# Optimization experiments

Hardware: AMD Instinct MI355X
Metric: run time of the kernel (lower is better)

## Reference

```python
import jax, jax.numpy as jnp
import numpy as np

B = 128          # batch of codewords
M_CHK = 288      # n_check_nodes
N_VAR = 576      # n_variable_nodes
K_INFO = 288     # n_information_bits
N_ITER = 5
EDGE_P = 0.02    # ~11-12 edges per check row, LDPC-like sparsity


def setup_inputs() -> dict:
    key = jax.random.key(0)
    k1, k2, k3, k4 = jax.random.split(key, 4)
    inputs = jax.random.normal(k1, (B, N_VAR), dtype=jnp.float32)
    # sparse binary parity-check matrix, batched (keras RNN constants carry batch dim)
    H = jax.random.bernoulli(k2, EDGE_P, (B, M_CHK, N_VAR)).astype(jnp.float32)
    sigma2 = 0.5 + 0.5 * jax.random.uniform(k3, (B, 1), dtype=jnp.float32)
    # learned parameters
    input_ponderation = jnp.ones((N_ITER, 1), dtype=jnp.float32)
    out_ponderation = jnp.ones((N_ITER, 1), dtype=jnp.float32)
    skip_ponderation = jnp.ones((1, 1), dtype=jnp.float32)
    # per-edge check-to-variable weights of the neural BP cell
    w_cv = 1.0 + 0.02 * jax.random.normal(k4, (M_CHK, N_VAR), dtype=jnp.float32)
    gate_logit = jnp.asarray(0.0, dtype=jnp.float32)
    return {"inputs": inputs, "H": H, "sigma2": sigma2,
            "input_ponderation": input_ponderation,
            "out_ponderation": out_ponderation,
            "skip_ponderation": skip_ponderation,
            "w_cv": w_cv, "gate_logit": gate_logit}


def _decode(inputs, H, sigma2, input_ponderation, out_ponderation,
            skip_ponderation, w_cv, gate_logit):
    llrs = -4.0 * inputs / sigma2                                    # [B, n]
    # trainable=True path: normalize by mean |llr|
    norm_llrs = llrs / jnp.mean(jnp.abs(llrs), axis=-1, keepdims=True)
    # tile over iterations and apply input ponderation -> [B, T, n]
    x = norm_llrs[:, None, :] * input_ponderation

    mask = H                                                         # [B, m, n]
    gate = jax.nn.sigmoid(gate_logit)

    def cell(Mstate, x_t):
        # variable-to-check extrinsic messages on edges
        S = jnp.sum(Mstate, axis=1, keepdims=True)                   # [B, 1, n]
        V = (x_t[:, None, :] + S - Mstate) * mask                    # [B, m, n]
        # tanh-product check-node update (product excluding self via divide)
        t = jnp.tanh(0.5 * jnp.clip(V, -15.0, 15.0))
        t_edge = jnp.where(mask > 0, t, 1.0)
        P = jnp.prod(t_edge, axis=-1, keepdims=True)                 # [B, m, 1]
        t_safe = jnp.where(jnp.abs(t_edge) < 1e-7,
                           jnp.where(t_edge >= 0, 1e-7, -1e-7), t_edge)
        r = jnp.clip(P / t_safe, -1.0 + 1e-6, 1.0 - 1e-6)
        M_new = 2.0 * jnp.arctanh(r) * w_cv * mask                   # weighted c2v
        # gated (damped) state update
        M_out = gate * M_new + (1.0 - gate) * Mstate
        posterior = x_t + jnp.sum(M_out, axis=1)                     # [B, n]
        return M_out, posterior

    M0 = jnp.zeros_like(H)
    xs = jnp.swapaxes(x, 0, 1)                                       # [T, B, n]
    _, posts = jax.lax.scan(cell, M0, xs)
    outputs = jnp.swapaxes(posts, 0, 1)                              # [B, T, n]

    # post-normalization per iteration, weighted pooling over iterations
    norm_out = outputs / jnp.mean(jnp.abs(outputs), axis=-1, keepdims=True)
    pooled = jnp.mean(out_ponderation * norm_out, axis=-2)           # [B, n]
    out = pooled + skip_ponderation * norm_llrs                      # [1,1] broadcast
    return jax.nn.sigmoid(-out[:, :K_INFO])


def reference(inputs, H, sigma2, input_ponderation, out_ponderation,
              skip_ponderation, w_cv, gate_logit):
    return _decode(inputs, H, sigma2, input_ponderation, out_ponderation,
                   skip_ponderation, w_cv, gate_logit)
```

## Files before the change

kernel.cpp:

```cpp
#include <hip/hip_runtime.h>

#define B_SZ  128
#define MCHK  288
#define NVAR  576
#define KINFO 288
#define NITER 5
#define ECAP  3712
#define CAP2  32
#define TPB   1024
#define NQ4   (MCHK * NVAR / 4)
#define Q4ROW (NVAR / 4)

__global__ __launch_bounds__(TPB) void decode(
    const float* __restrict__ inp,   const float* __restrict__ H,
    const float* __restrict__ sigma2,const float* __restrict__ ipond,
    const float* __restrict__ opond, const float* __restrict__ skipp,
    const float* __restrict__ wcv,   const float* __restrict__ gatel,
    float* __restrict__ out)
{
    __shared__ float Mld[ECAP];
    __shared__ float tld[ECAP];
    __shared__ float wld[ECAP];
    __shared__ unsigned int ev[ECAP];
    __shared__ float Sb[NITER + 1][NVAR];
    __shared__ float xln[NVAR];
    __shared__ float Prow[MCHK];
    __shared__ int   rcnt[MCHK], roff[MCHK];
    __shared__ unsigned short vpad[MCHK * CAP2];
    __shared__ float red[NITER * 16];
    __shared__ float scalv[NITER];
    __shared__ int   wtot[8], wbase[8];

    const int b    = blockIdx.x;
    const int tid  = threadIdx.x;
    const int wid  = tid >> 6;
    const int lane = tid & 63;

    const float sig  = sigma2[b];
    const float gate = 1.0f / (1.0f + __expf(-gatel[0]));
    const float gbar = 1.0f - gate;

    float ipl[NITER], opl[NITER];
    #pragma unroll
    for (int t = 0; t < NITER; ++t) { ipl[t] = ipond[t]; opl[t] = opond[t]; }

    float l = 0.0f, al = 0.0f, xv = 0.0f;
    if (tid < NVAR) { l = -4.0f * inp[(size_t)b * NVAR + tid] / sig; al = fabsf(l); }
    #pragma unroll
    for (int o = 32; o; o >>= 1) al += __shfl_down(al, o, 64);
    if (lane == 0) red[wid] = al;
    if (tid < MCHK) rcnt[tid] = 0;
    for (int i = tid; i < (NITER + 1) * NVAR; i += TPB) ((float*)Sb)[i] = 0.0f;
    __syncthreads();
    if (wid == 0) {
        float s = (lane < 16) ? red[lane] : 0.0f;
        s += __shfl_down(s, 8, 64); s += __shfl_down(s, 4, 64);
        s += __shfl_down(s, 2, 64); s += __shfl_down(s, 1, 64);
        if (lane == 0) scalv[0] = (float)NVAR / s;
    }
    __syncthreads();
    if (tid < NVAR) { xv = l * scalv[0]; xln[tid] = xv; }

    {
        const float4* H4 = (const float4*)(H + (size_t)b * MCHK * NVAR);
        for (int k = 0; k < (NQ4 + TPB - 1) / TPB; ++k) {
            int q = tid + k * TPB;
            if (q >= NQ4) break;
            float4 hv = H4[q];
            if (hv.x != 0.f || hv.y != 0.f || hv.z != 0.f || hv.w != 0.f) {
                int r  = q / Q4ROW;
                int c0 = (q - r * Q4ROW) * 4;
                unsigned short* vp = vpad + r * CAP2;
                if (hv.x != 0.f) { int j = atomicAdd(&rcnt[r], 1); if (j < CAP2) vp[j] = (unsigned short)(c0);     }
                if (hv.y != 0.f) { int j = atomicAdd(&rcnt[r], 1); if (j < CAP2) vp[j] = (unsigned short)(c0 + 1); }
                if (hv.z != 0.f) { int j = atomicAdd(&rcnt[r], 1); if (j < CAP2) vp[j] = (unsigned short)(c0 + 2); }
                if (hv.w != 0.f) { int j = atomicAdd(&rcnt[r], 1); if (j < CAP2) vp[j] = (unsigned short)(c0 + 3); }
            }
        }
    }
    __syncthreads();

    int cc = 0, incl = 0;
    if (tid < 512) {
        cc = (tid < MCHK) ? rcnt[tid] : 0;
        if (cc > CAP2) cc = CAP2;
        incl = cc;
        #pragma unroll
        for (int o = 1; o < 64; o <<= 1) {
            int n = __shfl_up(incl, o, 64);
            if (lane >= o) incl += n;
        }
        if (lane == 63) wtot[wid] = incl;
    }
    __syncthreads();
    if (tid == 0) {
        int s = 0;
        #pragma unroll
        for (int i = 0; i < 8; ++i) { wbase[i] = s; s += wtot[i]; }
    }
    __syncthreads();
    if (tid < MCHK) {
        int o = incl + wbase[wid] - cc;
        int ce = cc;
        if (o >= ECAP)           { o = 0; ce = 0; }
        else if (o + ce > ECAP)  { ce = ECAP - o; }
        roff[tid] = o; rcnt[tid] = ce;
    }
    const int Etot = wbase[7] + wtot[7];
    const int E    = (Etot > ECAP) ? ECAP : Etot;
    __syncthreads();

    for (int s = tid; s < MCHK * CAP2; s += TPB) {
        int r = s >> 5, j = s & (CAP2 - 1);
        if (j < rcnt[r]) {
            int e   = roff[r] + j;
            int col = vpad[s];
            ev[e]  = ((unsigned)r << 16) | (unsigned)col;
            wld[e] = wcv[r * NVAR + col];
            Mld[e] = 0.0f;
        }
    }
    __syncthreads();

    for (int t = 0; t < NITER; ++t) {
        const float pt = ipl[t];
        const float* St = Sb[t];
        float*       Sn = Sb[t + 1];

        for (int e = tid; e < E; e += TPB) {
            int v   = (int)(ev[e] & 0xFFFFu);
            float V = fmaf(pt, xln[v], St[v]) - Mld[e];
            V = fminf(15.0f, fmaxf(-15.0f, V));
            float ex = __expf(V);
            float te = (ex - 1.0f) * __builtin_amdgcn_rcpf(ex + 1.0f);
            float x  = 0.5f * V, x2 = x * x;
            float tp = x * fmaf(x2, fmaf(x2, fmaf(x2, -0.05396825f, 0.13333333f),
                                         -0.33333333f), 1.0f);
            tld[e] = (fabsf(V) < 0.5f) ? tp : te;
        }
        __syncthreads();

        if (tid < MCHK) {
            int o = roff[tid], oe = o + rcnt[tid];
            float p0 = 1.0f, p1 = 1.0f, p2 = 1.0f, p3 = 1.0f;
            int j = o;
            for (; j + 4 <= oe; j += 4) {
                float t0 = tld[j], t1 = tld[j + 1], t2 = tld[j + 2], t3 = tld[j + 3];
                p0 *= t0; p1 *= t1; p2 *= t2; p3 *= t3;
            }
            for (; j < oe; ++j) p0 *= tld[j];
            Prow[tid] = (p0 * p1) * (p2 * p3);
        }
        __syncthreads();

        for (int e = tid; e < E; e += TPB) {
            unsigned pk = ev[e];
            int v = (int)(pk & 0xFFFFu);
            int r = (int)(pk >> 16);
            float tj = tld[e];
            float ts = (fabsf(tj) < 1e-7f) ? ((tj >= 0.0f) ? 1e-7f : -1e-7f) : tj;
            float rr = Prow[r] * __builtin_amdgcn_rcpf(ts);
            rr = fminf(1.0f - 1e-6f, fmaxf(-1.0f + 1e-6f, rr));
            float Mn = __logf((1.0f + rr) * __builtin_amdgcn_rcpf(1.0f - rr)) * wld[e];
            float Mo = fmaf(gate, Mn, gbar * Mld[e]);
            Mld[e] = Mo;
            atomicAdd(&Sn[v], Mo);
        }
        __syncthreads();
    }

    float ap[NITER] = {0, 0, 0, 0, 0};
    if (tid < NVAR) {
        #pragma unroll
        for (int t = 0; t < NITER; ++t)
            ap[t] = fabsf(fmaf(ipl[t], xv, Sb[t + 1][tid]));
    }
    #pragma unroll
    for (int o = 32; o; o >>= 1) {
        #pragma unroll
        for (int t = 0; t < NITER; ++t) ap[t] += __shfl_down(ap[t], o, 64);
    }
    if (lane == 0) {
        #pragma unroll
        for (int t = 0; t < NITER; ++t) red[t * 16 + wid] = ap[t];
    }
    __syncthreads();
    if (wid == 0) {
        #pragma unroll
        for (int t = 0; t < NITER; ++t) {
            float s = (lane < 16) ? red[t * 16 + lane] : 0.0f;
            s += __shfl_down(s, 8, 64); s += __shfl_down(s, 4, 64);
            s += __shfl_down(s, 2, 64); s += __shfl_down(s, 1, 64);
            if (lane == 0) scalv[t] = (float)NVAR / s;
        }
    }
    __syncthreads();
    if (tid < KINFO) {
        float acc = 0.0f;
        #pragma unroll
        for (int t = 0; t < NITER; ++t)
            acc += opl[t] * fmaf(ipl[t], xv, Sb[t + 1][tid]) * scalv[t];
        float o = acc * (1.0f / NITER) + skipp[0] * xv;
        out[(size_t)b * KINFO + tid] = 1.0f / (1.0f + __expf(o));
    }
}

extern "C" void kernel_launch(void* const* d_in, const int* in_sizes, int n_in,
                              void* d_out, int out_size, void* d_ws, size_t ws_size,
                              hipStream_t stream) {
    const float* inp    = (const float*)d_in[0];
    const float* H      = (const float*)d_in[1];
    const float* sigma2 = (const float*)d_in[2];
    const float* ipond  = (const float*)d_in[3];
    const float* opond  = (const float*)d_in[4];
    const float* skipp  = (const float*)d_in[5];
    const float* wcv    = (const float*)d_in[6];
    const float* gatel  = (const float*)d_in[7];
    float* out = (float*)d_out;

    decode<<<B_SZ, TPB, 0, stream>>>(inp, H, sigma2, ipond, opond, skipp,
                                     wcv, gatel, out);
}
```

Measured before the change: 189.2 us.

## Split sparse edge extraction into wide kernel and use log-domain row products

Moves the dense scan of H (the dominant memory read) out of the 128-block decoder into a separate extraction kernel launched with 16 blocks per codeword, which writes compact edge lists to workspace. Edges of each row are no longer contiguous, so the per-row tanh product is computed in the log domain with shared-memory atomics for the log-magnitude sum and the negative-sign count. The extrinsic product is then recovered by exp2 of a difference, which replaces the serial per-row product loop and a barrier. This adds a memset, an extra launch, a global round-trip for the edges and atomic contention, and log-domain rounding differs slightly from the direct division.

```diff
diff --git a/kernel.cpp b/kernel.cpp
--- a/kernel.cpp
+++ b/kernel.cpp
@@ -5,31 +5,103 @@
 #define NVAR  576
 #define KINFO 288
 #define NITER 5
-#define ECAP  3712
+#define EPAD  4096
+#define RPB   18
+#define XBLK  (MCHK / RPB)
 #define CAP2  32
 #define TPB   1024
-#define NQ4   (MCHK * NVAR / 4)
-#define Q4ROW (NVAR / 4)
+
+__device__ __forceinline__ void scat(float4 hv, int q, int* rc,
+                                     unsigned short* vpad) {
+    if (hv.x != 0.f || hv.y != 0.f || hv.z != 0.f || hv.w != 0.f) {
+        int r  = q / (NVAR / 4);
+        int c0 = (q - r * (NVAR / 4)) * 4;
+        unsigned short* vp = vpad + r * CAP2;
+        if (hv.x != 0.f) { int j = atomicAdd(&rc[r], 1); if (j < CAP2) vp[j] = (unsigned short)(c0);     }
+        if (hv.y != 0.f) { int j = atomicAdd(&rc[r], 1); if (j < CAP2) vp[j] = (unsigned short)(c0 + 1); }
+        if (hv.z != 0.f) { int j = atomicAdd(&rc[r], 1); if (j < CAP2) vp[j] = (unsigned short)(c0 + 2); }
+        if (hv.w != 0.f) { int j = atomicAdd(&rc[r], 1); if (j < CAP2) vp[j] = (unsigned short)(c0 + 3); }
+    }
+}
+
+__global__ __launch_bounds__(256) void extract(
+    const float* __restrict__ H, const float* __restrict__ wcv,
+    int* __restrict__ eCnt, unsigned int* __restrict__ evG,
+    float* __restrict__ wG)
+{
+    __shared__ unsigned short vpad[RPB * CAP2];
+    __shared__ int rc[RPB], ro[RPB];
+    __shared__ int baseS;
+
+    const int b    = blockIdx.x >> 4;
+    const int g    = blockIdx.x & 15;
+    const int tid  = threadIdx.x;
+    const int row0 = g * RPB;
+
+    if (tid < RPB) rc[tid] = 0;
+    __syncthreads();
+
+    const float4* H4 = (const float4*)(H + ((size_t)b * MCHK + row0) * NVAR);
+    #pragma unroll
+    for (int k0 = 0; k0 < 8; k0 += 4) {
+        int q0 = tid + k0 * 256;
+        float4 h0 = H4[q0], h1 = H4[q0 + 256], h2 = H4[q0 + 512], h3 = H4[q0 + 768];
+        scat(h0, q0, rc, vpad);       scat(h1, q0 + 256, rc, vpad);
+        scat(h2, q0 + 512, rc, vpad); scat(h3, q0 + 768, rc, vpad);
+    }
+    {
+        int q0 = tid + 8 * 256;
+        float4 h0 = H4[q0], h1 = H4[q0 + 256];
+        scat(h0, q0, rc, vpad); scat(h1, q0 + 256, rc, vpad);
+    }
+    if (tid < 32) { int q = tid + 2560; scat(H4[q], q, rc, vpad); }
+    __syncthreads();
+
+    if (tid < 64) {
+        int c = (tid < RPB) ? ((rc[tid] > CAP2) ? CAP2 : rc[tid]) : 0;
+        int incl = c;
+        #pragma unroll
+        for (int o = 1; o < 64; o <<= 1) {
+            int n = __shfl_up(incl, o, 64);
+            if (tid >= o) incl += n;
+        }
+        if (tid < RPB) { ro[tid] = incl - c; rc[tid] = c; }
+        int tot = __shfl(incl, RPB - 1, 64);
+        if (tid == 0) baseS = atomicAdd(&eCnt[b], tot);
+    }
+    __syncthreads();
+    const int base = baseS;
+    for (int s = tid; s < RPB * CAP2; s += 256) {
+        int r = s >> 5, j = s & 31;
+        if (j < rc[r]) {
+            int e = base + ro[r] + j;
+            if (e < EPAD) {
+                int col  = vpad[s];
+                int grow = row0 + r;
+                evG[(size_t)b * EPAD + e] = ((unsigned)grow << 16) | (unsigned)col;
+                wG [(size_t)b * EPAD + e] = wcv[grow * NVAR + col];
+            }
+        }
+    }
+}
 
 __global__ __launch_bounds__(TPB) void decode(
-    const float* __restrict__ inp,   const float* __restrict__ H,
-    const float* __restrict__ sigma2,const float* __restrict__ ipond,
-    const float* __restrict__ opond, const float* __restrict__ skipp,
-    const float* __restrict__ wcv,   const float* __restrict__ gatel,
-    float* __restrict__ out)
+    const float* __restrict__ inp,   const float* __restrict__ sigma2,
+    const float* __restrict__ ipond, const float* __restrict__ opond,
+    const float* __restrict__ skipp, const float* __restrict__ gatel,
+    const int* __restrict__ eCnt,    const unsigned int* __restrict__ evG,
+    const float* __restrict__ wG,    float* __restrict__ out)
 {
-    __shared__ float Mld[ECAP];
-    __shared__ float tld[ECAP];
-    __shared__ float wld[ECAP];
-    __shared__ unsigned int ev[ECAP];
+    __shared__ unsigned int ev[EPAD];
+    __shared__ float wld[EPAD];
+    __shared__ float Mld[EPAD];
+    __shared__ float pld[EPAD];
     __shared__ float Sb[NITER + 1][NVAR];
     __shared__ float xln[NVAR];
-    __shared__ float Prow[MCHK];
-    __shared__ int   rcnt[MCHK], roff[MCHK];
-    __shared__ unsigned short vpad[MCHK * CAP2];
+    __shared__ float Plog[2][MCHK];
+    __shared__ int   Png [2][MCHK];
     __shared__ float red[NITER * 16];
     __shared__ float scalv[NITER];
-    __shared__ int   wtot[8], wbase[8];
 
     const int b    = blockIdx.x;
     const int tid  = threadIdx.x;
@@ -49,8 +121,18 @@
     #pragma unroll
     for (int o = 32; o; o >>= 1) al += __shfl_down(al, o, 64);
     if (lane == 0) red[wid] = al;
-    if (tid < MCHK) rcnt[tid] = 0;
     for (int i = tid; i < (NITER + 1) * NVAR; i += TPB) ((float*)Sb)[i] = 0.0f;
+    if (tid < 2 * MCHK) { ((float*)Plog)[tid] = 0.0f; ((int*)Png)[tid] = 0; }
+
+    const int E = min(eCnt[b], EPAD);
+    #pragma unroll
+    for (int k = 0; k < EPAD / TPB; ++k) {
+        int j = tid + k * TPB;
+        unsigned e = ((unsigned)MCHK << 16);
+        float w = 0.0f;
+        if (j < E) { e = evG[(size_t)b * EPAD + j]; w = wG[(size_t)b * EPAD + j]; }
+        ev[j] = e; wld[j] = w; Mld[j] = 0.0f;
+    }
     __syncthreads();
     if (wid == 0) {
         float s = (lane < 16) ? red[lane] : 0.0f;
@@ -60,112 +142,61 @@
     }
     __syncthreads();
     if (tid < NVAR) { xv = l * scalv[0]; xln[tid] = xv; }
-
-    {
-        const float4* H4 = (const float4*)(H + (size_t)b * MCHK * NVAR);
-        for (int k = 0; k < (NQ4 + TPB - 1) / TPB; ++k) {
-            int q = tid + k * TPB;
-            if (q >= NQ4) break;
-            float4 hv = H4[q];
-            if (hv.x != 0.f || hv.y != 0.f || hv.z != 0.f || hv.w != 0.f) {
-                int r  = q / Q4ROW;
-                int c0 = (q - r * Q4ROW) * 4;
-                unsigned short* vp = vpad + r * CAP2;
-                if (hv.x != 0.f) { int j = atomicAdd(&rcnt[r], 1); if (j < CAP2) vp[j] = (unsigned short)(c0);     }
-                if (hv.y != 0.f) { int j = atomicAdd(&rcnt[r], 1); if (j < CAP2) vp[j] = (unsigned short)(c0 + 1); }
-                if (hv.z != 0.f) { int j = atomicAdd(&rcnt[r], 1); if (j < CAP2) vp[j] = (unsigned short)(c0 + 2); }
-                if (hv.w != 0.f) { int j = atomicAdd(&rcnt[r], 1); if (j < CAP2) vp[j] = (unsigned short)(c0 + 3); }
-            }
-        }
-    }
-    __syncthreads();
-
-    int cc = 0, incl = 0;
-    if (tid < 512) {
-        cc = (tid < MCHK) ? rcnt[tid] : 0;
-        if (cc > CAP2) cc = CAP2;
-        incl = cc;
-        #pragma unroll
-        for (int o = 1; o < 64; o <<= 1) {
-            int n = __shfl_up(incl, o, 64);
-            if (lane >= o) incl += n;
-        }
-        if (lane == 63) wtot[wid] = incl;
-    }
-    __syncthreads();
-    if (tid == 0) {
-        int s = 0;
-        #pragma unroll
-        for (int i = 0; i < 8; ++i) { wbase[i] = s; s += wtot[i]; }
-    }
-    __syncthreads();
-    if (tid < MCHK) {
-        int o = incl + wbase[wid] - cc;
-        int ce = cc;
-        if (o >= ECAP)           { o = 0; ce = 0; }
-        else if (o + ce > ECAP)  { ce = ECAP - o; }
-        roff[tid] = o; rcnt[tid] = ce;
-    }
-    const int Etot = wbase[7] + wtot[7];
-    const int E    = (Etot > ECAP) ? ECAP : Etot;
-    __syncthreads();
-
-    for (int s = tid; s < MCHK * CAP2; s += TPB) {
-        int r = s >> 5, j = s & (CAP2 - 1);
-        if (j < rcnt[r]) {
-            int e   = roff[r] + j;
-            int col = vpad[s];
-            ev[e]  = ((unsigned)r << 16) | (unsigned)col;
-            wld[e] = wcv[r * NVAR + col];
-            Mld[e] = 0.0f;
-        }
-    }
     __syncthreads();
 
     for (int t = 0; t < NITER; ++t) {
+        const int cur = t & 1, nxt = cur ^ 1;
         const float pt = ipl[t];
         const float* St = Sb[t];
         float*       Sn = Sb[t + 1];
 
-        for (int e = tid; e < E; e += TPB) {
-            int v   = (int)(ev[e] & 0xFFFFu);
-            float V = fmaf(pt, xln[v], St[v]) - Mld[e];
-            V = fminf(15.0f, fmaxf(-15.0f, V));
-            float ex = __expf(V);
-            float te = (ex - 1.0f) * __builtin_amdgcn_rcpf(ex + 1.0f);
-            float x  = 0.5f * V, x2 = x * x;
-            float tp = x * fmaf(x2, fmaf(x2, fmaf(x2, -0.05396825f, 0.13333333f),
-                                         -0.33333333f), 1.0f);
-            tld[e] = (fabsf(V) < 0.5f) ? tp : te;
+        #pragma unroll
+        for (int k = 0; k < EPAD / TPB; ++k) {
+            int e = tid + k * TPB;
+            unsigned pk = ev[e];
+            int r = (int)(pk >> 16);
+            if (r < MCHK) {
+                int v = (int)(pk & 0xFFFFu);
+                float V = fmaf(pt, xln[v], St[v]) - Mld[e];
+                V = fminf(15.0f, fmaxf(-15.0f, V));
+                float ex = __expf(V);
+                float te = (ex - 1.0f) * __builtin_amdgcn_rcpf(ex + 1.0f);
+                float x  = 0.5f * V, x2 = x * x;
+                float tp = x * fmaf(x2, fmaf(x2, fmaf(x2, -0.05396825f, 0.13333333f),
+                                             -0.33333333f), 1.0f);
+                float tt = (fabsf(V) < 0.5f) ? tp : te;
+                float lg = __builtin_amdgcn_logf(fabsf(tt));
+                pld[e] = __builtin_copysignf(fabsf(lg), tt);
+                atomicAdd(&Plog[cur][r], lg);
+                if (tt < 0.0f) atomicAdd(&Png[cur][r], 1);
+            }
         }
         __syncthreads();
 
-        if (tid < MCHK) {
-            int o = roff[tid], oe = o + rcnt[tid];
-            float p0 = 1.0f, p1 = 1.0f, p2 = 1.0f, p3 = 1.0f;
-            int j = o;
-            for (; j + 4 <= oe; j += 4) {
-                float t0 = tld[j], t1 = tld[j + 1], t2 = tld[j + 2], t3 = tld[j + 3];
-                p0 *= t0; p1 *= t1; p2 *= t2; p3 *= t3;
+        #pragma unroll
+        for (int k = 0; k < EPAD / TPB; ++k) {
+            int e = tid + k * TPB;
+            unsigned pk = ev[e];
+            int r = (int)(pk >> 16);
+            if (r < MCHK) {
+                int v = (int)(pk & 0xFFFFu);
+                float pe  = pld[e];
+                float lg  = -fabsf(pe);
+                float lgs = fmaxf(lg, -23.2534966f);
+                float mag = __builtin_amdgcn_exp2f(Plog[cur][r] - lgs);
+                int   neg = (Png[cur][r] + (__builtin_signbitf(pe) ? 1 : 0)) & 1;
+                float rr  = fminf(mag, 1.0f - 1e-6f);
+                rr = neg ? -rr : rr;
+                float Mn = 0.69314718f *
+                           __builtin_amdgcn_logf((1.0f + rr) *
+                                                 __builtin_amdgcn_rcpf(1.0f - rr)) *
+                           wld[e];
+                float Mo = fmaf(gate, Mn, gbar * Mld[e]);
+                Mld[e] = Mo;
+                atomicAdd(&Sn[v], Mo);
             }
-            for (; j < oe; ++j) p0 *= tld[j];
-            Prow[tid] = (p0 * p1) * (p2 * p3);
-        }
-        __syncthreads();
-
-        for (int e = tid; e < E; e += TPB) {
-            unsigned pk = ev[e];
-            int v = (int)(pk & 0xFFFFu);
-            int r = (int)(pk >> 16);
-            float tj = tld[e];
-            float ts = (fabsf(tj) < 1e-7f) ? ((tj >= 0.0f) ? 1e-7f : -1e-7f) : tj;
-            float rr = Prow[r] * __builtin_amdgcn_rcpf(ts);
-            rr = fminf(1.0f - 1e-6f, fmaxf(-1.0f + 1e-6f, rr));
-            float Mn = __logf((1.0f + rr) * __builtin_amdgcn_rcpf(1.0f - rr)) * wld[e];
-            float Mo = fmaf(gate, Mn, gbar * Mld[e]);
-            Mld[e] = Mo;
-            atomicAdd(&Sn[v], Mo);
-        }
+        }
+        if (tid < MCHK) { Plog[nxt][tid] = 0.0f; Png[nxt][tid] = 0; }
         __syncthreads();
     }
 
@@ -218,6 +249,12 @@
     const float* gatel  = (const float*)d_in[7];
     float* out = (float*)d_out;
 
-    decode<<<B_SZ, TPB, 0, stream>>>(inp, H, sigma2, ipond, opond, skipp,
-                                     wcv, gatel, out);
-}
+    int*          eCnt = (int*)d_ws;
+    unsigned int* evG  = (unsigned int*)((char*)d_ws + 4096);
+    float*        wG   = (float*)((char*)d_ws + 4096 + (size_t)B_SZ * EPAD * 4);
+
+    hipMemsetAsync(eCnt, 0, B_SZ * sizeof(int), stream);
+    extract<<<B_SZ * XBLK, 256, 0, stream>>>(H, wcv, eCnt, evG, wG);
+    decode<<<B_SZ, TPB, 0, stream>>>(inp, sigma2, ipond, opond, skipp,
+                                     gatel, eCnt, evG, wG, out);
+}
```

Measured after the change: 206.5 us. +9.1%, slower.
